# Kernel optimization log

Measured on AMD Instinct MI355X. Metric: run time of the kernel, lower is better.

The kernel has to match this reference:

```python
import jax, jax.numpy as jnp
import numpy as np

HEAD_DIM = 32
KS = 3            # kernel_size
DIL = 2           # dilation
PAD = DIL * (KS - 1) // 2
SCALE = HEAD_DIM ** (-0.5)


def _unfold(x):
    """nn.ReflectionPad2d(PAD) + nn.Unfold(KS, dilation=DIL).
    x: [B, C, H, W] -> [B, C, KS*KS, H, W] with kernel positions row-major,
    matching nn.Unfold's (C, kh, kw) channel ordering."""
    B, C, H, W = x.shape
    xp = jnp.pad(x, ((0, 0), (0, 0), (PAD, PAD), (PAD, PAD)), mode='reflect')
    patches = jnp.stack(
        [xp[:, :, i * DIL:i * DIL + H, j * DIL:j * DIL + W]
         for i in range(KS) for j in range(KS)],
        axis=2,
    )
    return patches  # [B, C, ksq, H, W]


def setup_inputs() -> dict:
    key = jax.random.key(0)
    kq, kk, kv = jax.random.split(key, 3)
    shape = (16, 384, 56, 56)
    return {
        'q': jax.random.normal(kq, shape, dtype=jnp.float32),
        'k': jax.random.normal(kk, shape, dtype=jnp.float32),
        'v': jax.random.normal(kv, shape, dtype=jnp.float32),
    }


def reference(q, k, v):
    B, d, H, W = q.shape
    nH = d // HEAD_DIM
    ksq = KS * KS
    # q: [B, nH, headDim, H, W]
    q_r = q.reshape(B, nH, HEAD_DIM, H, W)
    # k/v unfolded: [B, nH, headDim, ksq, H, W]
    k_p = _unfold(k).reshape(B, nH, HEAD_DIM, ksq, H, W)
    v_p = _unfold(v).reshape(B, nH, HEAD_DIM, ksq, H, W)
    # attention scores over the ksq local window
    attn = jnp.einsum('bnchw,bnckhw->bnkhw', q_r, k_p) * SCALE
    attn = jax.nn.softmax(attn, axis=2)
    out = jnp.einsum('bnkhw,bnckhw->bnchw', attn, v_p)
    # [B, nH, headDim, H, W] -> [B, H, W, nH*headDim]
    out = out.reshape(B, d, H, W).transpose(0, 2, 3, 1)
    return out
```

## Files before the change

### kernel.cpp

```cpp
#include <hip/hip_runtime.h>
#include <stdint.h>


#define BB 16
#define CH 384
#define HH 56
#define WW 56
#define NH 12
#define DD 32
#define HW (HH * WW)
#define KSQ 9
#define SCALE 0.17677669529663687f

#define BAND 8
#define DCH 8
#define NCHUNK (DD / DCH)
#define MAXROWS 12
#define SLICE (MAXROWS * WW)
#define LBUF (DCH * SLICE)

__device__ __forceinline__ void async16(const void* g, void* l) {
    __builtin_amdgcn_global_load_lds(
        (const __attribute__((address_space(1))) void*)g,
        (__attribute__((address_space(3))) void*)l, 16, 0, 0);
}

__device__ __forceinline__ void stage_chunk(const float* __restrict__ plane0,
                                            float* ldsbuf, int Sbytes,
                                            int wv, int lane) {
    const int lo16 = lane * 16;
    for (int s = wv; s < DCH; s += 7) {
        const char* g = (const char*)(plane0 + s * HW);
        char* l = (char*)(ldsbuf + s * SLICE);
        async16(g + lo16, l + lo16);
        async16(g + 1024 + lo16, l + 1024 + lo16);
        const int t = Sbytes - 1024;
        async16(g + t + lo16, l + t + lo16);
    }
}

__global__ __launch_bounds__(448, 5)
void dilate_attn_kernel(const float* __restrict__ q,
                        const float* __restrict__ k,
                        const float* __restrict__ v,
                        float* __restrict__ out) {
    __shared__ float lds[2][LBUF];

    const int band = blockIdx.x;
    const int n    = blockIdx.y;
    const int b    = blockIdx.z;

    const int tid  = threadIdx.x;
    const int lane = tid & 63;
    const int wv   = tid >> 6;

    const int w = tid % WW;
    const int r = tid / WW;
    const int h0 = band * BAND;
    const int h  = h0 + r;

    const int lo = (h0 - 2 < 0) ? 0 : h0 - 2;
    const int hi = (h0 + 9 > HH - 1) ? HH - 1 : h0 + 9;
    const int Sbytes = (hi - lo + 1) * WW * 4;

    int off9[KSQ];
    {
        int wc[3];
#pragma unroll
        for (int j = 0; j < 3; ++j) {
            int c = w + 2 * (j - 1);
            c = (c < 0) ? -c : ((c >= WW) ? (2 * WW - 2 - c) : c);
            wc[j] = c;
        }
#pragma unroll
        for (int i = 0; i < 3; ++i) {
            int rr = h + 2 * (i - 1);
            rr = (rr < 0) ? -rr : ((rr >= HH) ? (2 * HH - 2 - rr) : rr);
            rr -= lo;
#pragma unroll
            for (int j = 0; j < 3; ++j) off9[i * 3 + j] = rr * WW + wc[j];
        }
    }

    const int planebase = (b * CH + n * DD) * HW;
    const float* qp = q + planebase + h * WW + w;
    const float* kstage = k + planebase + lo * WW;
    const float* vstage = v + planebase + lo * WW;

    float sc[KSQ];
#pragma unroll
    for (int ii = 0; ii < KSQ; ++ii) sc[ii] = 0.f;

    stage_chunk(kstage, lds[0], Sbytes, wv, lane);
    __syncthreads();
    int cur = 0;

    for (int c = 0; c < NCHUNK; ++c) {
        if (c < NCHUNK - 1)
            stage_chunk(kstage + (c + 1) * DCH * HW, lds[cur ^ 1], Sbytes, wv, lane);
        else
            stage_chunk(vstage, lds[cur ^ 1], Sbytes, wv, lane);

        float qd[DCH];
#pragma unroll
        for (int j = 0; j < DCH; ++j) qd[j] = qp[(c * DCH + j) * HW];

        const float* Bf = lds[cur];
#pragma unroll
        for (int j = 0; j < DCH; ++j) {
            const float* Ls = Bf + j * SLICE;
            const float qj = qd[j];
#pragma unroll
            for (int ii = 0; ii < KSQ; ++ii)
                sc[ii] = fmaf(qj, Ls[off9[ii]], sc[ii]);
        }
        __syncthreads();
        cur ^= 1;
    }

    {
        float m = sc[0];
#pragma unroll
        for (int ii = 1; ii < KSQ; ++ii) m = fmaxf(m, sc[ii]);
        float sum = 0.f;
#pragma unroll
        for (int ii = 0; ii < KSQ; ++ii) {
            sc[ii] = __expf((sc[ii] - m) * SCALE);
            sum += sc[ii];
        }
        const float inv = 1.f / sum;
#pragma unroll
        for (int ii = 0; ii < KSQ; ++ii) sc[ii] *= inv;
    }

    float* op = out + ((b * HH + h) * WW + w) * CH + n * DD;

    for (int c = 0; c < NCHUNK; ++c) {
        if (c < NCHUNK - 1)
            stage_chunk(vstage + (c + 1) * DCH * HW, lds[cur ^ 1], Sbytes, wv, lane);

        const float* Bf = lds[cur];
        float o[DCH];
#pragma unroll
        for (int j = 0; j < DCH; ++j) {
            const float* Ls = Bf + j * SLICE;
            float acc = 0.f;
#pragma unroll
            for (int ii = 0; ii < KSQ; ++ii)
                acc = fmaf(sc[ii], Ls[off9[ii]], acc);
            o[j] = acc;
        }
        *(float4*)(op + c * DCH)     = make_float4(o[0], o[1], o[2], o[3]);
        *(float4*)(op + c * DCH + 4) = make_float4(o[4], o[5], o[6], o[7]);

        if (c < NCHUNK - 1) {
            __syncthreads();
            cur ^= 1;
        }
    }
}

extern "C" void kernel_launch(void* const* d_in, const int* in_sizes, int n_in,
                              void* d_out, int out_size, void* d_ws, size_t ws_size,
                              hipStream_t stream) {
    const float* q = (const float*)d_in[0];
    const float* k = (const float*)d_in[1];
    const float* v = (const float*)d_in[2];
    float* out = (float*)d_out;

    dim3 grid(HH / BAND, NH, BB);
    dilate_attn_kernel<<<grid, 448, 0, stream>>>(q, k, v, out);
}
```

Before: 280.3 us.

## Restructure pipeline to one row per wave with manual vmcnt waits and prefetch

Each block now runs 512 threads: 8 waves, one image row per wave, with lanes past 56 idle. Staging is restructured into a depth-two prefetch that keeps two chunks in flight. It uses explicit s_waitcnt vmcnt counts and raw s_barrier in place of __syncthreads, and the q values for the next chunk are prefetched into registers. The aim is to hide global-to-LDS load latency and avoid full waits at every barrier. In exchange, 8 of every 64 lanes sit idle, and correctness depends on hand-counted vmcnt values.

Measured after the change: 276.9 us. No clear change (-1.2%).

```diff
diff --git a/kernel.cpp b/kernel.cpp
--- a/kernel.cpp
+++ b/kernel.cpp
@@ -19,6 +19,10 @@
 #define SLICE (MAXROWS * WW)
 #define LBUF (DCH * SLICE)
 
+#define WAITV(n) asm volatile("s_waitcnt vmcnt(" #n ")" ::: "memory")
+#define FENCE()  asm volatile("" ::: "memory")
+#define BAR()    do { FENCE(); __builtin_amdgcn_s_barrier(); FENCE(); } while (0)
+
 __device__ __forceinline__ void async16(const void* g, void* l) {
     __builtin_amdgcn_global_load_lds(
         (const __attribute__((address_space(1))) void*)g,
@@ -29,22 +33,20 @@
                                             float* ldsbuf, int Sbytes,
                                             int wv, int lane) {
     const int lo16 = lane * 16;
-    for (int s = wv; s < DCH; s += 7) {
-        const char* g = (const char*)(plane0 + s * HW);
-        char* l = (char*)(ldsbuf + s * SLICE);
-        async16(g + lo16, l + lo16);
-        async16(g + 1024 + lo16, l + 1024 + lo16);
-        const int t = Sbytes - 1024;
-        async16(g + t + lo16, l + t + lo16);
-    }
+    const char* g = (const char*)(plane0 + wv * HW);
+    char* l = (char*)(ldsbuf + wv * SLICE);
+    async16(g + lo16, l + lo16);
+    async16(g + 1024 + lo16, l + 1024 + lo16);
+    const int t = Sbytes - 1024;
+    async16(g + t + lo16, l + t + lo16);
 }
 
-__global__ __launch_bounds__(448, 5)
+__global__ __launch_bounds__(512, 6)
 void dilate_attn_kernel(const float* __restrict__ q,
                         const float* __restrict__ k,
                         const float* __restrict__ v,
                         float* __restrict__ out) {
-    __shared__ float lds[2][LBUF];
+    __shared__ __align__(16) float lds[2][LBUF];
 
     const int band = blockIdx.x;
     const int n    = blockIdx.y;
@@ -54,10 +56,10 @@
     const int lane = tid & 63;
     const int wv   = tid >> 6;
 
-    const int w = tid % WW;
-    const int r = tid / WW;
+    const bool act = lane < WW;
+    const int w  = act ? lane : (WW - 1);
     const int h0 = band * BAND;
-    const int h  = h0 + r;
+    const int h  = h0 + wv;
 
     const int lo = (h0 - 2 < 0) ? 0 : h0 - 2;
     const int hi = (h0 + 9 > HH - 1) ? HH - 1 : h0 + 9;
@@ -92,20 +94,24 @@
     for (int ii = 0; ii < KSQ; ++ii) sc[ii] = 0.f;
 
     stage_chunk(kstage, lds[0], Sbytes, wv, lane);
-    __syncthreads();
-    int cur = 0;
+    FENCE();
+    float qd[DCH];
+#pragma unroll
+    for (int j = 0; j < DCH; ++j) qd[j] = qp[j * HW];
+    FENCE();
+    stage_chunk(kstage + DCH * HW, lds[1], Sbytes, wv, lane);
+    FENCE();
 
+#pragma unroll
     for (int c = 0; c < NCHUNK; ++c) {
-        if (c < NCHUNK - 1)
-            stage_chunk(kstage + (c + 1) * DCH * HW, lds[cur ^ 1], Sbytes, wv, lane);
-        else
-            stage_chunk(vstage, lds[cur ^ 1], Sbytes, wv, lane);
-
-        float qd[DCH];
+        WAITV(11);
+        BAR();
+        float qn[DCH];
+        if (c < NCHUNK - 1) {
 #pragma unroll
-        for (int j = 0; j < DCH; ++j) qd[j] = qp[(c * DCH + j) * HW];
-
-        const float* Bf = lds[cur];
+            for (int j = 0; j < DCH; ++j) qn[j] = qp[((c + 1) * DCH + j) * HW];
+        }
+        const float* Bf = lds[c & 1];
 #pragma unroll
         for (int j = 0; j < DCH; ++j) {
             const float* Ls = Bf + j * SLICE;
@@ -114,8 +120,16 @@
             for (int ii = 0; ii < KSQ; ++ii)
                 sc[ii] = fmaf(qj, Ls[off9[ii]], sc[ii]);
         }
-        __syncthreads();
-        cur ^= 1;
+        if (c < NCHUNK - 1) {
+#pragma unroll
+            for (int j = 0; j < DCH; ++j) qd[j] = qn[j];
+        }
+        BAR();
+        const float* src = (c + 2 < NCHUNK)
+                               ? (kstage + (c + 2) * DCH * HW)
+                               : (vstage + (c + 2 - NCHUNK) * DCH * HW);
+        stage_chunk(src, lds[c & 1], Sbytes, wv, lane);
+        FENCE();
     }
 
     {
@@ -135,11 +149,13 @@
 
     float* op = out + ((b * HH + h) * WW + w) * CH + n * DD;
 
-    for (int c = 0; c < NCHUNK; ++c) {
-        if (c < NCHUNK - 1)
-            stage_chunk(vstage + (c + 1) * DCH * HW, lds[cur ^ 1], Sbytes, wv, lane);
-
-        const float* Bf = lds[cur];
+#pragma unroll
+    for (int p = 0; p < NCHUNK; ++p) {
+        if (p == 0)      WAITV(3);
+        else if (p == 3) WAITV(2);
+        else             WAITV(5);
+        BAR();
+        const float* Bf = lds[p & 1];
         float o[DCH];
 #pragma unroll
         for (int j = 0; j < DCH; ++j) {
@@ -150,12 +166,14 @@
                 acc = fmaf(sc[ii], Ls[off9[ii]], acc);
             o[j] = acc;
         }
-        *(float4*)(op + c * DCH)     = make_float4(o[0], o[1], o[2], o[3]);
-        *(float4*)(op + c * DCH + 4) = make_float4(o[4], o[5], o[6], o[7]);
-
-        if (c < NCHUNK - 1) {
-            __syncthreads();
-            cur ^= 1;
+        if (act) {
+            *(float4*)(op + p * DCH)     = make_float4(o[0], o[1], o[2], o[3]);
+            *(float4*)(op + p * DCH + 4) = make_float4(o[4], o[5], o[6], o[7]);
+        }
+        if (p < 2) {
+            BAR();
+            stage_chunk(vstage + (p + 2) * DCH * HW, lds[p & 1], Sbytes, wv, lane);
+            FENCE();
         }
     }
 }
@@ -169,5 +187,5 @@
     float* out = (float*)d_out;
 
     dim3 grid(HH / BAND, NH, BB);
-    dilate_attn_kernel<<<grid, 448, 0, stream>>>(q, k, v, out);
+    dilate_attn_kernel<<<grid, 512, 0, stream>>>(q, k, v, out);
 }
```
